# Kernel optimization log

Measured on AMD Instinct MI355X. Metric: run time of the kernel, lower is better.

The kernel has to match this reference:

```python
import jax, jax.numpy as jnp
import numpy as np

NEG_SLOPE = 0.2

def gat_conv(x, src, dst, W, a_src, a_dst, bias, num_nodes, heads, out_ch, concat):
    # x: [N, Fin]; W: [Fin, heads*out_ch]; a_src/a_dst: [heads, out_ch]
    h = (x @ W).reshape(num_nodes, heads, out_ch)            # [N,H,C]
    alpha_s = jnp.einsum('nhc,hc->nh', h, a_src)             # [N,H]
    alpha_d = jnp.einsum('nhc,hc->nh', h, a_dst)             # [N,H]
    e = alpha_s[src] + alpha_d[dst]                          # [E,H]
    e = jnp.where(e > 0, e, NEG_SLOPE * e)                   # LeakyReLU
    # segment softmax over incoming edges per destination node
    m = jax.ops.segment_max(e, dst, num_segments=num_nodes)  # [N,H]
    m = jnp.where(jnp.isfinite(m), m, 0.0)
    ee = jnp.exp(e - m[dst])                                 # [E,H]
    s = jax.ops.segment_sum(ee, dst, num_segments=num_nodes) # [N,H]
    alpha = ee / (s[dst] + 1e-16)                            # [E,H]
    out = jax.ops.segment_sum(h[src] * alpha[:, :, None], dst,
                              num_segments=num_nodes)        # [N,H,C]
    if concat:
        out = out.reshape(num_nodes, heads * out_ch)
    else:
        out = out.mean(axis=1)
    return out + bias


def setup_inputs() -> dict:
    key = jax.random.key(0)
    ks = jax.random.split(key, 10)
    N, E = 50000, 800000
    EMB, HID, HEADS, REPR = 128, 128, 8, 64
    C1 = HID // HEADS  # 16
    x = jax.random.normal(ks[0], (N, EMB), dtype=jnp.float32)
    edge_index = jax.random.randint(ks[1], (2, E), 0, N, dtype=jnp.int32)
    sc = 1.0 / np.sqrt(EMB)
    W1 = jax.random.normal(ks[2], (EMB, HEADS * C1), dtype=jnp.float32) * sc
    a1_src = jax.random.normal(ks[3], (HEADS, C1), dtype=jnp.float32) * 0.1
    a1_dst = jax.random.normal(ks[4], (HEADS, C1), dtype=jnp.float32) * 0.1
    b1 = jnp.zeros((HID,), dtype=jnp.float32)
    sc2 = 1.0 / np.sqrt(HID)
    W2 = jax.random.normal(ks[5], (HID, REPR), dtype=jnp.float32) * sc2
    a2_src = jax.random.normal(ks[6], (1, REPR), dtype=jnp.float32) * 0.1
    a2_dst = jax.random.normal(ks[7], (1, REPR), dtype=jnp.float32) * 0.1
    b2 = jnp.zeros((REPR,), dtype=jnp.float32)
    return {"x": x, "edge_index": edge_index,
            "W1": W1, "a1_src": a1_src, "a1_dst": a1_dst, "b1": b1,
            "W2": W2, "a2_src": a2_src, "a2_dst": a2_dst, "b2": b2}


def reference(x, edge_index, W1, a1_src, a1_dst, b1, W2, a2_src, a2_dst, b2):
    N = x.shape[0]
    # PyG GATConv adds self-loops by default
    loops = jnp.arange(N, dtype=edge_index.dtype)
    src = jnp.concatenate([edge_index[0], loops])
    dst = jnp.concatenate([edge_index[1], loops])
    # eval mode: F.dropout(p=0.6) is identity
    h = gat_conv(x, src, dst, W1, a1_src, a1_dst, b1, N,
                 heads=8, out_ch=16, concat=True)
    h = jax.nn.elu(h)
    out = gat_conv(h, src, dst, W2, a2_src, a2_dst, b2, N,
                   heads=1, out_ch=64, concat=True)
    return out
```

## Files before the change

kernel.cpp:

```cpp
#include <hip/hip_runtime.h>
#include <hip/hip_fp16.h>
#include <math.h>


typedef _Float16 f16x8 __attribute__((ext_vector_type(8)));
typedef float f32x4 __attribute__((ext_vector_type(4)));

#define PAD 16

__device__ __forceinline__ float leaky_exp(float e) {
    e = (e > 0.f) ? e : 0.2f * e;
    return __expf(e);
}

__device__ __forceinline__ void acc16(float w, float4 hv0, float4 hv1,
                                      float* __restrict__ acc) {
    const __half2* p0 = (const __half2*)&hv0;
    const __half2* p1 = (const __half2*)&hv1;
#pragma unroll
    for (int k = 0; k < 4; k++) {
        float2 f = __half22float2(p0[k]);
        acc[2 * k] += w * f.x;
        acc[2 * k + 1] += w * f.y;
    }
#pragma unroll
    for (int k = 0; k < 4; k++) {
        float2 f = __half22float2(p1[k]);
        acc[8 + 2 * k] += w * f.x;
        acc[8 + 2 * k + 1] += w * f.y;
    }
}

__device__ __forceinline__ void acc8(float w, float4 hv,
                                     float* __restrict__ acc) {
    const __half2* hp = (const __half2*)&hv;
#pragma unroll
    for (int k = 0; k < 4; k++) {
        float2 f = __half22float2(hp[k]);
        acc[2 * k] += w * f.x;
        acc[2 * k + 1] += w * f.y;
    }
}

__global__ __launch_bounds__(256) void augw_hist_kernel(
        const float* __restrict__ W1, const float* __restrict__ a1s,
        const float* __restrict__ a1d, const float* __restrict__ W2,
        const float* __restrict__ a2s, const float* __restrict__ a2d,
        _Float16* __restrict__ W1t, _Float16* __restrict__ W2t,
        const int* __restrict__ src, const int* __restrict__ dst,
        int E, int N, int* __restrict__ deg8,
        int* __restrict__ bucketCnt, int2* __restrict__ pairs) {
    __shared__ int lcnt[8];
    __shared__ int lbase[8];
    int t = threadIdx.x;
    if (blockIdx.x == 0) {
        for (int i = t; i < 144 * 128; i += 256) {
            int c = i >> 7, k = i & 127;
            float v;
            if (c < 128) {
                v = W1[k * 128 + c];
            } else if (c < 136) {
                int h = c - 128; v = 0.f;
#pragma unroll
                for (int j = 0; j < 16; j++) v += W1[k * 128 + h * 16 + j] * a1s[h * 16 + j];
            } else {
                int h = c - 136; v = 0.f;
#pragma unroll
                for (int j = 0; j < 16; j++) v += W1[k * 128 + h * 16 + j] * a1d[h * 16 + j];
            }
            W1t[c * 128 + k] = (_Float16)v;
        }
        return;
    }
    if (blockIdx.x == 1) {
        for (int i = t; i < 80 * 128; i += 256) {
            int c = i >> 7, k = i & 127;
            float v = 0.f;
            if (c < 64) {
                v = W2[k * 64 + c];
            } else if (c == 64) {
                for (int j = 0; j < 64; j++) v += W2[k * 64 + j] * a2s[j];
            } else if (c == 65) {
                for (int j = 0; j < 64; j++) v += W2[k * 64 + j] * a2d[j];
            }
            W2t[c * 128 + k] = (_Float16)v;
        }
        return;
    }
    if (t < 8) lcnt[t] = 0;
    __syncthreads();
    int bid = blockIdx.x - 2;
    int c = bid & 7;
    int bdiv = (N + 7) >> 3;
    int i0 = (bid * 256 + t) * 4;
    int s_[4], d_[4], bk[4], rk[4];
    int nv = 0;
    if (i0 + 3 < E) {
        int4 d4 = *(const int4*)(dst + i0);
        int4 s4 = *(const int4*)(src + i0);
        s_[0] = s4.x; s_[1] = s4.y; s_[2] = s4.z; s_[3] = s4.w;
        d_[0] = d4.x; d_[1] = d4.y; d_[2] = d4.z; d_[3] = d4.w;
        nv = 4;
    } else {
        for (int k = i0; k < E && nv < 4; k++) {
            s_[nv] = src[k]; d_[nv] = dst[k]; nv++;
        }
    }
    int lane = t & 63;
    unsigned long long below = (lane == 0) ? 0ULL : (~0ULL >> (64 - lane));
#pragma unroll
    for (int u = 0; u < 4; u++) {
        bool v = (u < nv);
        int d = v ? d_[u] : 0;
        if (v) atomicAdd(&deg8[d * 8 + c], 1);
        int b = d / bdiv;
        unsigned long long m0 = __ballot(b & 1);
        unsigned long long m1 = __ballot(b & 2);
        unsigned long long m2 = __ballot(b & 4);
        unsigned long long vm = __ballot(v);
        unsigned long long me = ((b & 1) ? m0 : ~m0) & ((b & 2) ? m1 : ~m1) &
                                ((b & 4) ? m2 : ~m2) & vm;
        int leader = __ffsll((unsigned long long)me) - 1;
        int ldr = (leader < 0) ? 0 : leader;
        int cnt = __popcll(me);
        int rank = __popcll(me & below);
        int base = 0;
        if (v && lane == leader) base = atomicAdd(&lcnt[b], cnt);
        base = __shfl(base, ldr);
        bk[u] = b;
        rk[u] = base + rank;
    }
    __syncthreads();
    if (t < 8) lbase[t] = atomicAdd(&bucketCnt[t * 16], lcnt[t]);
    __syncthreads();
#pragma unroll 4
    for (int k = 0; k < nv; k++) {
        pairs[(size_t)bk[k] * E + lbase[bk[k]] + rk[k]] = make_int2(s_[k], d_[k]);
    }
}

__global__ __launch_bounds__(256) void scan1_kernel(const int* __restrict__ deg8, int N,
                                                    int* __restrict__ rowstart,
                                                    int* __restrict__ blocksum) {
    __shared__ int tmp[256];
    int t = threadIdx.x;
    int i = blockIdx.x * 256 + t;
    int v = 0;
    if (i < N) {
        int4 a = *(const int4*)(deg8 + i * 8);
        int4 b = *(const int4*)(deg8 + i * 8 + 4);
        v = a.x + a.y + a.z + a.w + b.x + b.y + b.z + b.w;
    }
    tmp[t] = v;
    __syncthreads();
    for (int off = 1; off < 256; off <<= 1) {
        int x = (t >= off) ? tmp[t - off] : 0;
        __syncthreads();
        tmp[t] += x;
        __syncthreads();
    }
    if (i < N) rowstart[i] = tmp[t] - v;
    if (t == 255) blocksum[blockIdx.x] = tmp[t];
}

__global__ __launch_bounds__(256) void scan23_kernel(int* __restrict__ rowstart,
                                                     const int* __restrict__ blocksum,
                                                     int nb,
                                                     int* __restrict__ cursor,
                                                     int N, int E) {
    __shared__ int sdata[256];
    int t = threadIdx.x;
    int b = blockIdx.x;
    sdata[t] = (t < nb && t < b) ? blocksum[t] : 0;
    __syncthreads();
#pragma unroll
    for (int off = 128; off > 0; off >>= 1) {
        if (t < off) sdata[t] += sdata[t + off];
        __syncthreads();
    }
    int offset = sdata[0];
    int i = b * 256 + t;
    if (i < N) {
        int v = rowstart[i] + offset;
        rowstart[i] = v;
        cursor[i * PAD] = v;
    } else if (i == N) {
        rowstart[N] = E;
    }
}

__global__ __launch_bounds__(256) void gemm1_scatter_kernel(
        const float* __restrict__ x, const _Float16* __restrict__ W1t,
        __half* __restrict__ h1, float* __restrict__ als,
        float* __restrict__ ald, int N, int gridG1,
        const int* __restrict__ bucketCnt, const int2* __restrict__ pairs,
        int E, int nChunk,
        int* __restrict__ cursor, int* __restrict__ esrc) {
    __shared__ _Float16 Xs[64 * 136];
    int t = threadIdx.x;
    if ((int)blockIdx.x >= gridG1) {
        int sbid = blockIdx.x - gridG1;
        int b = sbid & 7;
        int chunk = sbid >> 3;
        int cnt = bucketCnt[b * 16];
        const int2* plist = pairs + (size_t)b * E;
        for (int ii = chunk * 1024; ii < cnt; ii += nChunk * 1024) {
#pragma unroll
            for (int u = 0; u < 4; u++) {
                int i = ii + u * 256 + t;
                if (i < cnt) {
                    int2 p = plist[i];
                    int pos = atomicAdd(&cursor[p.y * PAD], 1);
                    esrc[pos] = p.x;
                }
            }
        }
        return;
    }
    int row0 = blockIdx.x * 64;
    for (int i = t; i < 2048; i += 256) {
        int r = i >> 5, c4 = i & 31;
        int gr = row0 + r;
        float4 v = make_float4(0.f, 0.f, 0.f, 0.f);
        if (gr < N) v = *(const float4*)(x + (size_t)gr * 128 + c4 * 4);
        _Float16* dp = Xs + r * 136 + c4 * 4;
        dp[0] = (_Float16)v.x; dp[1] = (_Float16)v.y;
        dp[2] = (_Float16)v.z; dp[3] = (_Float16)v.w;
    }
    __syncthreads();
    int w = t >> 6, L = t & 63, m = L & 15, quad = L >> 4;
    f32x4 acc[9];
#pragma unroll
    for (int f = 0; f < 9; f++) acc[f] = (f32x4){0.f, 0.f, 0.f, 0.f};
    const _Float16* Arow = Xs + (w * 16 + m) * 136 + quad * 8;
    const _Float16* Brow = W1t + m * 128 + quad * 8;
#pragma unroll
    for (int kt = 0; kt < 4; kt++) {
        f16x8 a = *(const f16x8*)(Arow + kt * 32);
#pragma unroll
        for (int f = 0; f < 9; f++) {
            f16x8 b = *(const f16x8*)(Brow + f * 2048 + kt * 32);
            acc[f] = __builtin_amdgcn_mfma_f32_16x16x32_f16(a, b, acc[f], 0, 0, 0);
        }
    }
    int nbase = row0 + w * 16 + quad * 4;
#pragma unroll
    for (int r = 0; r < 4; r++) {
        int n = nbase + r;
        if (n < N) {
            __half* hrow = h1 + (size_t)n * 128 + m;
#pragma unroll
            for (int f = 0; f < 8; f++) hrow[f * 16] = __float2half(acc[f][r]);
            float v = acc[8][r];
            if (m < 8) als[n * 8 + m] = v;
            else ald[n * 8 + (m - 8)] = v;
        }
    }
}

__global__ __launch_bounds__(256) void agg1_kernel(const __half* __restrict__ h1,
                                                   const float* __restrict__ als,
                                                   const float* __restrict__ ald,
                                                   const int* __restrict__ rowstart,
                                                   const int* __restrict__ esrc,
                                                   const float* __restrict__ b1,
                                                   __half* __restrict__ act1, int N) {
    int t = threadIdx.x;
    int lane = t & 63;
    int grp = lane >> 3;
    int q = lane & 7;
    int bdiv = (N + 7) >> 3;
    int ln = (blockIdx.x >> 3) * 32 + (t >> 6) * 8 + grp;
    if (ln >= bdiv) return;
    int n = (blockIdx.x & 7) * bdiv + ln;
    if (n >= N) return;
    const float4* h1v = (const float4*)h1;
    float adv = ald[n * 8 + q];
    float acc[16];
#pragma unroll
    for (int k = 0; k < 16; k++) acc[k] = 0.f;
    float wsum = 0.f;
    {
        float w = leaky_exp(als[n * 8 + q] + adv);
        wsum += w;
        acc16(w, h1v[(size_t)n * 16 + 2 * q], h1v[(size_t)n * 16 + 2 * q + 1], acc);
    }
    int beg = rowstart[n], end = rowstart[n + 1];
    int j = beg;
    for (; j + 4 <= end; j += 4) {
        int s0 = esrc[j], s1 = esrc[j + 1], s2 = esrc[j + 2], s3 = esrc[j + 3];
        float4 a0 = h1v[(size_t)s0 * 16 + 2 * q], b0 = h1v[(size_t)s0 * 16 + 2 * q + 1];
        float4 a1 = h1v[(size_t)s1 * 16 + 2 * q], b1 = h1v[(size_t)s1 * 16 + 2 * q + 1];
        float4 a2 = h1v[(size_t)s2 * 16 + 2 * q], b2 = h1v[(size_t)s2 * 16 + 2 * q + 1];
        float4 a3 = h1v[(size_t)s3 * 16 + 2 * q], b3 = h1v[(size_t)s3 * 16 + 2 * q + 1];
        float e0 = als[s0 * 8 + q], e1 = als[s1 * 8 + q];
        float e2 = als[s2 * 8 + q], e3 = als[s3 * 8 + q];
        float w0 = leaky_exp(e0 + adv), w1 = leaky_exp(e1 + adv);
        float w2 = leaky_exp(e2 + adv), w3 = leaky_exp(e3 + adv);
        wsum += (w0 + w1) + (w2 + w3);
        acc16(w0, a0, b0, acc);
        acc16(w1, a1, b1, acc);
        acc16(w2, a2, b2, acc);
        acc16(w3, a3, b3, acc);
    }
    for (; j < end; j++) {
        int s = esrc[j];
        float w = leaky_exp(als[s * 8 + q] + adv);
        wsum += w;
        acc16(w, h1v[(size_t)s * 16 + 2 * q], h1v[(size_t)s * 16 + 2 * q + 1], acc);
    }
    float inv = 1.f / (wsum + 1e-16f);
    const float* bf = b1 + q * 16;
    __align__(16) __half2 po[8];
#pragma unroll
    for (int k = 0; k < 8; k++) {
        float o0 = acc[2 * k] * inv + bf[2 * k];
        float o1 = acc[2 * k + 1] * inv + bf[2 * k + 1];
        o0 = (o0 > 0.f) ? o0 : (__expf(o0) - 1.f);
        o1 = (o1 > 0.f) ? o1 : (__expf(o1) - 1.f);
        po[k] = __floats2half2_rn(o0, o1);
    }
    float4* ov = (float4*)(act1 + (size_t)n * 128 + q * 16);
    ov[0] = ((float4*)po)[0];
    ov[1] = ((float4*)po)[1];
}

__global__ __launch_bounds__(256) void gemm2_kernel(const __half* __restrict__ act1,
                                                    const _Float16* __restrict__ W2t,
                                                    __half* __restrict__ h2,
                                                    float* __restrict__ al2s,
                                                    float* __restrict__ al2d, int N) {
    int t = threadIdx.x;
    int row0 = blockIdx.x * 64;
    int w = t >> 6, L = t & 63, m = L & 15, quad = L >> 4;
    f32x4 acc[5];
#pragma unroll
    for (int f = 0; f < 5; f++) acc[f] = (f32x4){0.f, 0.f, 0.f, 0.f};
    const _Float16* Arow =
        (const _Float16*)act1 + (size_t)(row0 + w * 16 + m) * 128 + quad * 8;
    const _Float16* Brow = W2t + m * 128 + quad * 8;
#pragma unroll
    for (int kt = 0; kt < 4; kt++) {
        f16x8 a = *(const f16x8*)(Arow + kt * 32);
#pragma unroll
        for (int f = 0; f < 5; f++) {
            f16x8 b = *(const f16x8*)(Brow + f * 2048 + kt * 32);
            acc[f] = __builtin_amdgcn_mfma_f32_16x16x32_f16(a, b, acc[f], 0, 0, 0);
        }
    }
    int nbase = row0 + w * 16 + quad * 4;
#pragma unroll
    for (int r = 0; r < 4; r++) {
        int n = nbase + r;
        if (n < N) {
            __half* hrow = h2 + (size_t)n * 64 + m;
#pragma unroll
            for (int f = 0; f < 4; f++) hrow[f * 16] = __float2half(acc[f][r]);
            if (m == 0) al2s[n] = acc[4][r];
            else if (m == 1) al2d[n] = acc[4][r];
        }
    }
}

__global__ __launch_bounds__(256) void agg2_kernel(const __half* __restrict__ h2,
                                                   const float* __restrict__ al2s,
                                                   const float* __restrict__ al2d,
                                                   const int* __restrict__ rowstart,
                                                   const int* __restrict__ esrc,
                                                   const float* __restrict__ b2,
                                                   float* __restrict__ out, int N) {
    int t = threadIdx.x;
    int lane = t & 63;
    int grp = lane >> 3;
    int q = lane & 7;
    int bdiv = (N + 7) >> 3;
    int ln = (blockIdx.x >> 3) * 32 + (t >> 6) * 8 + grp;
    if (ln >= bdiv) return;
    int n = (blockIdx.x & 7) * bdiv + ln;
    if (n >= N) return;
    const float4* h2v = (const float4*)h2;
    float adv = al2d[n];
    float acc[8];
#pragma unroll
    for (int k = 0; k < 8; k++) acc[k] = 0.f;
    float wsum = 0.f;
    {
        float w = leaky_exp(al2s[n] + adv);
        wsum += w;
        acc8(w, h2v[(size_t)n * 8 + q], acc);
    }
    int beg = rowstart[n], end = rowstart[n + 1];
    int j = beg;
    for (; j + 4 <= end; j += 4) {
        int s0 = esrc[j], s1 = esrc[j + 1], s2 = esrc[j + 2], s3 = esrc[j + 3];
        float4 a0 = h2v[(size_t)s0 * 8 + q];
        float4 a1 = h2v[(size_t)s1 * 8 + q];
        float4 a2 = h2v[(size_t)s2 * 8 + q];
        float4 a3 = h2v[(size_t)s3 * 8 + q];
        float e0 = al2s[s0], e1 = al2s[s1], e2 = al2s[s2], e3 = al2s[s3];
        float w0 = leaky_exp(e0 + adv), w1 = leaky_exp(e1 + adv);
        float w2 = leaky_exp(e2 + adv), w3 = leaky_exp(e3 + adv);
        wsum += (w0 + w1) + (w2 + w3);
        acc8(w0, a0, acc);
        acc8(w1, a1, acc);
        acc8(w2, a2, acc);
        acc8(w3, a3, acc);
    }
    for (; j < end; j++) {
        int s = esrc[j];
        float w = leaky_exp(al2s[s] + adv);
        wsum += w;
        acc8(w, h2v[(size_t)s * 8 + q], acc);
    }
    float inv = 1.f / (wsum + 1e-16f);
    const float* bf = b2 + q * 8;
    float4* ov = (float4*)(out + (size_t)n * 64 + q * 8);
    ov[0] = make_float4(acc[0] * inv + bf[0], acc[1] * inv + bf[1],
                        acc[2] * inv + bf[2], acc[3] * inv + bf[3]);
    ov[1] = make_float4(acc[4] * inv + bf[4], acc[5] * inv + bf[5],
                        acc[6] * inv + bf[6], acc[7] * inv + bf[7]);
}

extern "C" void kernel_launch(void* const* d_in, const int* in_sizes, int n_in,
                              void* d_out, int out_size, void* d_ws, size_t ws_size,
                              hipStream_t stream) {
    (void)n_in; (void)out_size; (void)ws_size;
    const float* x   = (const float*)d_in[0];
    const int*   ei  = (const int*)d_in[1];
    const float* W1  = (const float*)d_in[2];
    const float* a1s = (const float*)d_in[3];
    const float* a1d = (const float*)d_in[4];
    const float* b1  = (const float*)d_in[5];
    const float* W2  = (const float*)d_in[6];
    const float* a2s = (const float*)d_in[7];
    const float* a2d = (const float*)d_in[8];
    const float* b2  = (const float*)d_in[9];
    float* out = (float*)d_out;

    const int N = in_sizes[0] / 128;
    const int E = in_sizes[1] / 2;
    const int* src = ei;
    const int* dst = ei + E;

    char* wp = (char*)d_ws;
    auto alloc = [&](size_t bytes) -> void* {
        void* p = (void*)wp;
        wp += (bytes + 255) & ~(size_t)255;
        return p;
    };
    __half* h1   = (__half*)alloc((size_t)N * 128 * 2);
    __half* act1 = (__half*)alloc((size_t)N * 128 * 2);
    __half* h2   = (__half*)alloc((size_t)N * 64 * 2 + 64 * 256);
    float* al1s = (float*)alloc((size_t)N * 8 * 4);
    float* al1d = (float*)alloc((size_t)N * 8 * 4);
    float* al2s = (float*)alloc((size_t)N * 4);
    float* al2d = (float*)alloc((size_t)N * 4);
    int* deg8     = (int*)alloc((size_t)N * 8 * 4);
    int* bucketCnt = (int*)alloc(8 * 16 * 4);
    int* rowstart = (int*)alloc((size_t)(N + 1) * 4);
    int* cursor   = (int*)alloc((size_t)N * PAD * 4);
    int* esrc     = (int*)alloc((size_t)E * 4);
    int2* pairs   = (int2*)alloc((size_t)8 * E * 8);
    int* blocksum = (int*)alloc(256 * 4);
    _Float16* W1t = (_Float16*)alloc(144 * 128 * 2);
    _Float16* W2t = (_Float16*)alloc(80 * 128 * 2);

    const int nbScan = (N + 255) / 256;
    const int gridH  = (E + 1023) / 1024;
    const int gridG1 = (N + 63) / 64;
    const int gridG2 = (N + 63) / 64;
    const int bdiv = (N + 7) / 8;
    const int gridAggN = 8 * ((bdiv + 31) / 32);
    const int nChunk = ((E + 7) / 8 + 1023) / 1024 + 2;
    const int gridScat = 8 * nChunk;

    hipMemsetAsync(deg8, 0, (size_t)N * 8 * 4 + 8 * 16 * 4, stream);

    augw_hist_kernel<<<2 + gridH, 256, 0, stream>>>(W1, a1s, a1d, W2, a2s, a2d,
                                                    W1t, W2t, src, dst, E, N,
                                                    deg8, bucketCnt, pairs);
    scan1_kernel<<<nbScan, 256, 0, stream>>>(deg8, N, rowstart, blocksum);
    scan23_kernel<<<(N + 256) / 256, 256, 0, stream>>>(rowstart, blocksum, nbScan,
                                                       cursor, N, E);
    gemm1_scatter_kernel<<<gridG1 + gridScat, 256, 0, stream>>>(
        x, W1t, h1, al1s, al1d, N, gridG1, bucketCnt, pairs, E, nChunk,
        cursor, esrc);

    agg1_kernel<<<gridAggN, 256, 0, stream>>>(h1, al1s, al1d, rowstart, esrc, b1, act1, N);
    gemm2_kernel<<<gridG2, 256, 0, stream>>>(act1, W2t, h2, al2s, al2d, N);
    agg2_kernel<<<gridAggN, 256, 0, stream>>>(h2, al2s, al2d, rowstart, esrc, b2, out, N);
}
```

Before: 258.9 us.

## Overlap GEMM1 with edge histogram and split scatter into its own kernel

Reschedules the pipeline so the edge histogram and bucketing run alongside the first GEMM in one launch, instead of being fused with the weight-augmentation prep. The scatter into CSR now runs as a separate kernel after the scans. The per-node degree counter is collapsed from 8 striped copies to a single int per node, which shrinks the memset and the scan reads but concentrates atomics on one address per node. It adds an extra kernel launch and changes which work overlaps.

```diff
diff --git a/kernel.cpp b/kernel.cpp
--- a/kernel.cpp
+++ b/kernel.cpp
@@ -42,16 +42,14 @@
     }
 }
 
-__global__ __launch_bounds__(256) void augw_hist_kernel(
-        const float* __restrict__ W1, const float* __restrict__ a1s,
-        const float* __restrict__ a1d, const float* __restrict__ W2,
-        const float* __restrict__ a2s, const float* __restrict__ a2d,
-        _Float16* __restrict__ W1t, _Float16* __restrict__ W2t,
-        const int* __restrict__ src, const int* __restrict__ dst,
-        int E, int N, int* __restrict__ deg8,
-        int* __restrict__ bucketCnt, int2* __restrict__ pairs) {
-    __shared__ int lcnt[8];
-    __shared__ int lbase[8];
+__global__ __launch_bounds__(256) void augw_kernel(const float* __restrict__ W1,
+                                                   const float* __restrict__ a1s,
+                                                   const float* __restrict__ a1d,
+                                                   const float* __restrict__ W2,
+                                                   const float* __restrict__ a2s,
+                                                   const float* __restrict__ a2d,
+                                                   _Float16* __restrict__ W1t,
+                                                   _Float16* __restrict__ W2t) {
     int t = threadIdx.x;
     if (blockIdx.x == 0) {
         for (int i = t; i < 144 * 128; i += 256) {
@@ -70,9 +68,7 @@
             }
             W1t[c * 128 + k] = (_Float16)v;
         }
-        return;
-    }
-    if (blockIdx.x == 1) {
+    } else {
         for (int i = t; i < 80 * 128; i += 256) {
             int c = i >> 7, k = i & 127;
             float v = 0.f;
@@ -85,135 +81,69 @@
             }
             W2t[c * 128 + k] = (_Float16)v;
         }
-        return;
-    }
-    if (t < 8) lcnt[t] = 0;
-    __syncthreads();
-    int bid = blockIdx.x - 2;
-    int c = bid & 7;
-    int bdiv = (N + 7) >> 3;
-    int i0 = (bid * 256 + t) * 4;
-    int s_[4], d_[4], bk[4], rk[4];
-    int nv = 0;
-    if (i0 + 3 < E) {
-        int4 d4 = *(const int4*)(dst + i0);
-        int4 s4 = *(const int4*)(src + i0);
-        s_[0] = s4.x; s_[1] = s4.y; s_[2] = s4.z; s_[3] = s4.w;
-        d_[0] = d4.x; d_[1] = d4.y; d_[2] = d4.z; d_[3] = d4.w;
-        nv = 4;
-    } else {
-        for (int k = i0; k < E && nv < 4; k++) {
-            s_[nv] = src[k]; d_[nv] = dst[k]; nv++;
-        }
-    }
-    int lane = t & 63;
-    unsigned long long below = (lane == 0) ? 0ULL : (~0ULL >> (64 - lane));
-#pragma unroll
-    for (int u = 0; u < 4; u++) {
-        bool v = (u < nv);
-        int d = v ? d_[u] : 0;
-        if (v) atomicAdd(&deg8[d * 8 + c], 1);
-        int b = d / bdiv;
-        unsigned long long m0 = __ballot(b & 1);
-        unsigned long long m1 = __ballot(b & 2);
-        unsigned long long m2 = __ballot(b & 4);
-        unsigned long long vm = __ballot(v);
-        unsigned long long me = ((b & 1) ? m0 : ~m0) & ((b & 2) ? m1 : ~m1) &
-                                ((b & 4) ? m2 : ~m2) & vm;
-        int leader = __ffsll((unsigned long long)me) - 1;
-        int ldr = (leader < 0) ? 0 : leader;
-        int cnt = __popcll(me);
-        int rank = __popcll(me & below);
-        int base = 0;
-        if (v && lane == leader) base = atomicAdd(&lcnt[b], cnt);
-        base = __shfl(base, ldr);
-        bk[u] = b;
-        rk[u] = base + rank;
-    }
-    __syncthreads();
-    if (t < 8) lbase[t] = atomicAdd(&bucketCnt[t * 16], lcnt[t]);
-    __syncthreads();
-#pragma unroll 4
-    for (int k = 0; k < nv; k++) {
-        pairs[(size_t)bk[k] * E + lbase[bk[k]] + rk[k]] = make_int2(s_[k], d_[k]);
-    }
-}
-
-__global__ __launch_bounds__(256) void scan1_kernel(const int* __restrict__ deg8, int N,
-                                                    int* __restrict__ rowstart,
-                                                    int* __restrict__ blocksum) {
-    __shared__ int tmp[256];
-    int t = threadIdx.x;
-    int i = blockIdx.x * 256 + t;
-    int v = 0;
-    if (i < N) {
-        int4 a = *(const int4*)(deg8 + i * 8);
-        int4 b = *(const int4*)(deg8 + i * 8 + 4);
-        v = a.x + a.y + a.z + a.w + b.x + b.y + b.z + b.w;
-    }
-    tmp[t] = v;
-    __syncthreads();
-    for (int off = 1; off < 256; off <<= 1) {
-        int x = (t >= off) ? tmp[t - off] : 0;
-        __syncthreads();
-        tmp[t] += x;
-        __syncthreads();
-    }
-    if (i < N) rowstart[i] = tmp[t] - v;
-    if (t == 255) blocksum[blockIdx.x] = tmp[t];
-}
-
-__global__ __launch_bounds__(256) void scan23_kernel(int* __restrict__ rowstart,
-                                                     const int* __restrict__ blocksum,
-                                                     int nb,
-                                                     int* __restrict__ cursor,
-                                                     int N, int E) {
-    __shared__ int sdata[256];
-    int t = threadIdx.x;
-    int b = blockIdx.x;
-    sdata[t] = (t < nb && t < b) ? blocksum[t] : 0;
-    __syncthreads();
-#pragma unroll
-    for (int off = 128; off > 0; off >>= 1) {
-        if (t < off) sdata[t] += sdata[t + off];
-        __syncthreads();
-    }
-    int offset = sdata[0];
-    int i = b * 256 + t;
-    if (i < N) {
-        int v = rowstart[i] + offset;
-        rowstart[i] = v;
-        cursor[i * PAD] = v;
-    } else if (i == N) {
-        rowstart[N] = E;
-    }
-}
-
-__global__ __launch_bounds__(256) void gemm1_scatter_kernel(
+    }
+}
+
+__global__ __launch_bounds__(256) void gemm1_hist_kernel(
         const float* __restrict__ x, const _Float16* __restrict__ W1t,
         __half* __restrict__ h1, float* __restrict__ als,
         float* __restrict__ ald, int N, int gridG1,
-        const int* __restrict__ bucketCnt, const int2* __restrict__ pairs,
-        int E, int nChunk,
-        int* __restrict__ cursor, int* __restrict__ esrc) {
+        const int* __restrict__ src, const int* __restrict__ dst, int E,
+        int* __restrict__ deg, int* __restrict__ bucketCnt,
+        int2* __restrict__ pairs) {
     __shared__ _Float16 Xs[64 * 136];
     int t = threadIdx.x;
     if ((int)blockIdx.x >= gridG1) {
-        int sbid = blockIdx.x - gridG1;
-        int b = sbid & 7;
-        int chunk = sbid >> 3;
-        int cnt = bucketCnt[b * 16];
-        const int2* plist = pairs + (size_t)b * E;
-        for (int ii = chunk * 1024; ii < cnt; ii += nChunk * 1024) {
-#pragma unroll
-            for (int u = 0; u < 4; u++) {
-                int i = ii + u * 256 + t;
-                if (i < cnt) {
-                    int2 p = plist[i];
-                    int pos = atomicAdd(&cursor[p.y * PAD], 1);
-                    esrc[pos] = p.x;
-                }
+        int* lcnt = (int*)Xs;
+        int* lbase = lcnt + 8;
+        if (t < 8) lcnt[t] = 0;
+        __syncthreads();
+        int bid = blockIdx.x - gridG1;
+        int bdiv = (N + 7) >> 3;
+        int i0 = (bid * 256 + t) * 4;
+        int s_[4], d_[4], bk[4], rk[4];
+        int nv = 0;
+        if (i0 + 3 < E) {
+            int4 d4 = *(const int4*)(dst + i0);
+            int4 s4 = *(const int4*)(src + i0);
+            s_[0] = s4.x; s_[1] = s4.y; s_[2] = s4.z; s_[3] = s4.w;
+            d_[0] = d4.x; d_[1] = d4.y; d_[2] = d4.z; d_[3] = d4.w;
+            nv = 4;
+        } else {
+            for (int k = i0; k < E && nv < 4; k++) {
+                s_[nv] = src[k]; d_[nv] = dst[k]; nv++;
             }
+        }
+        int lane = t & 63;
+        unsigned long long below = (lane == 0) ? 0ULL : (~0ULL >> (64 - lane));
+#pragma unroll
+        for (int u = 0; u < 4; u++) {
+            bool v = (u < nv);
+            int d = v ? d_[u] : 0;
+            if (v) atomicAdd(&deg[d], 1);
+            int b = d / bdiv;
+            unsigned long long m0 = __ballot(b & 1);
+            unsigned long long m1 = __ballot(b & 2);
+            unsigned long long m2 = __ballot(b & 4);
+            unsigned long long vm = __ballot(v);
+            unsigned long long me = ((b & 1) ? m0 : ~m0) & ((b & 2) ? m1 : ~m1) &
+                                    ((b & 4) ? m2 : ~m2) & vm;
+            int leader = __ffsll((unsigned long long)me) - 1;
+            int ldr = (leader < 0) ? 0 : leader;
+            int cnt = __popcll(me);
+            int rank = __popcll(me & below);
+            int base = 0;
+            if (v && lane == leader) base = atomicAdd(&lcnt[b], cnt);
+            base = __shfl(base, ldr);
+            bk[u] = b;
+            rk[u] = base + rank;
+        }
+        __syncthreads();
+        if (t < 8) lbase[t] = atomicAdd(&bucketCnt[t * 16], lcnt[t]);
+        __syncthreads();
+#pragma unroll 4
+        for (int k = 0; k < nv; k++) {
+            pairs[(size_t)bk[k] * E + lbase[bk[k]] + rk[k]] = make_int2(s_[k], d_[k]);
         }
         return;
     }
@@ -254,6 +184,72 @@
             float v = acc[8][r];
             if (m < 8) als[n * 8 + m] = v;
             else ald[n * 8 + (m - 8)] = v;
+        }
+    }
+}
+
+__global__ __launch_bounds__(256) void scan1_kernel(const int* __restrict__ deg, int N,
+                                                    int* __restrict__ rowstart,
+                                                    int* __restrict__ blocksum) {
+    __shared__ int tmp[256];
+    int t = threadIdx.x;
+    int i = blockIdx.x * 256 + t;
+    int v = (i < N) ? deg[i] : 0;
+    tmp[t] = v;
+    __syncthreads();
+    for (int off = 1; off < 256; off <<= 1) {
+        int x = (t >= off) ? tmp[t - off] : 0;
+        __syncthreads();
+        tmp[t] += x;
+        __syncthreads();
+    }
+    if (i < N) rowstart[i] = tmp[t] - v;
+    if (t == 255) blocksum[blockIdx.x] = tmp[t];
+}
+
+__global__ __launch_bounds__(256) void scan23_kernel(int* __restrict__ rowstart,
+                                                     const int* __restrict__ blocksum,
+                                                     int nb,
+                                                     int* __restrict__ cursor,
+                                                     int N, int E) {
+    __shared__ int sdata[256];
+    int t = threadIdx.x;
+    int b = blockIdx.x;
+    sdata[t] = (t < nb && t < b) ? blocksum[t] : 0;
+    __syncthreads();
+#pragma unroll
+    for (int off = 128; off > 0; off >>= 1) {
+        if (t < off) sdata[t] += sdata[t + off];
+        __syncthreads();
+    }
+    int offset = sdata[0];
+    int i = b * 256 + t;
+    if (i < N) {
+        int v = rowstart[i] + offset;
+        rowstart[i] = v;
+        cursor[i * PAD] = v;
+    } else if (i == N) {
+        rowstart[N] = E;
+    }
+}
+
+__global__ __launch_bounds__(256) void scatterB_kernel(
+        const int* __restrict__ bucketCnt, const int2* __restrict__ pairs,
+        int E, int nChunk, int* __restrict__ cursor, int* __restrict__ esrc) {
+    int t = threadIdx.x;
+    int b = blockIdx.x & 7;
+    int chunk = blockIdx.x >> 3;
+    int cnt = bucketCnt[b * 16];
+    const int2* plist = pairs + (size_t)b * E;
+    for (int ii = chunk * 1024; ii < cnt; ii += nChunk * 1024) {
+#pragma unroll
+        for (int u = 0; u < 4; u++) {
+            int i = ii + u * 256 + t;
+            if (i < cnt) {
+                int2 p = plist[i];
+                int pos = atomicAdd(&cursor[p.y * PAD], 1);
+                esrc[pos] = p.x;
+            }
         }
     }
 }
@@ -455,7 +451,8 @@
     float* al1d = (float*)alloc((size_t)N * 8 * 4);
     float* al2s = (float*)alloc((size_t)N * 4);
     float* al2d = (float*)alloc((size_t)N * 4);
-    int* deg8     = (int*)alloc((size_t)N * 8 * 4);
+    const size_t degBytesPadded = (((size_t)N * 4) + 255) & ~(size_t)255;
+    int* deg      = (int*)alloc((size_t)N * 4);
     int* bucketCnt = (int*)alloc(8 * 16 * 4);
     int* rowstart = (int*)alloc((size_t)(N + 1) * 4);
     int* cursor   = (int*)alloc((size_t)N * PAD * 4);
@@ -474,17 +471,16 @@
     const int nChunk = ((E + 7) / 8 + 1023) / 1024 + 2;
     const int gridScat = 8 * nChunk;
 
-    hipMemsetAsync(deg8, 0, (size_t)N * 8 * 4 + 8 * 16 * 4, stream);
-
-    augw_hist_kernel<<<2 + gridH, 256, 0, stream>>>(W1, a1s, a1d, W2, a2s, a2d,
-                                                    W1t, W2t, src, dst, E, N,
-                                                    deg8, bucketCnt, pairs);
-    scan1_kernel<<<nbScan, 256, 0, stream>>>(deg8, N, rowstart, blocksum);
+    hipMemsetAsync(deg, 0, degBytesPadded + 8 * 16 * 4, stream);
+
+    augw_kernel<<<2, 256, 0, stream>>>(W1, a1s, a1d, W2, a2s, a2d, W1t, W2t);
+    gemm1_hist_kernel<<<gridG1 + gridH, 256, 0, stream>>>(
+        x, W1t, h1, al1s, al1d, N, gridG1, src, dst, E, deg, bucketCnt, pairs);
+    scan1_kernel<<<nbScan, 256, 0, stream>>>(deg, N, rowstart, blocksum);
     scan23_kernel<<<(N + 256) / 256, 256, 0, stream>>>(rowstart, blocksum, nbScan,
                                                        cursor, N, E);
-    gemm1_scatter_kernel<<<gridG1 + gridScat, 256, 0, stream>>>(
-        x, W1t, h1, al1s, al1d, N, gridG1, bucketCnt, pairs, E, nChunk,
-        cursor, esrc);
+    scatterB_kernel<<<gridScat, 256, 0, stream>>>(bucketCnt, pairs, E, nChunk,
+                                                  cursor, esrc);
 
     agg1_kernel<<<gridAggN, 256, 0, stream>>>(h1, al1s, al1d, rowstart, esrc, b1, act1, N);
     gemm2_kernel<<<gridG2, 256, 0, stream>>>(act1, W2t, h2, al2s, al2d, N);
```

Result: slower. 275.2 us (+6.3%).
